# Optimization experiments

Measured on AMD Instinct MI355X. Metric: run time of the kernel, lower is better.

## Reference

```python
import jax, jax.numpy as jnp
import numpy as np
from jax import lax

B, C, H, W = 2, 384, 32, 32
N_HEAD, N_GROUP = 12, 6
HC = C // N_HEAD          # 32 head channels
GC = C // N_GROUP         # 64 group channels
GH = N_HEAD // N_GROUP    # 2 heads per group
KK = 7                    # depthwise kernel (25<=32<=48)
OFF_FACTOR = 2.0
SCALE = HC ** -0.5
EPS = 1e-5


def setup_inputs() -> dict:
    key = jax.random.key(0)
    ks = jax.random.split(key, 16)
    s = 0.02
    inp = {
        "x": jax.random.normal(ks[0], (B, C, H, W), jnp.float32),
        "Wq": jax.random.normal(ks[1], (C, C), jnp.float32) * s,
        "bq": jnp.zeros((C,), jnp.float32),
        "Wk": jax.random.normal(ks[2], (C, C), jnp.float32) * s,
        "bk": jnp.zeros((C,), jnp.float32),
        "Wv": jax.random.normal(ks[3], (C, C), jnp.float32) * s,
        "bv": jnp.zeros((C,), jnp.float32),
        "Wo": jax.random.normal(ks[4], (C, C), jnp.float32) * s,
        "bo": jnp.zeros((C,), jnp.float32),
        "off_dw_w": jax.random.normal(ks[5], (GC, 1, KK, KK), jnp.float32) * s,  # depthwise OIHW
        "off_dw_b": jnp.zeros((GC,), jnp.float32),
        "ln_g": jnp.ones((GC,), jnp.float32),
        "ln_b": jnp.zeros((GC,), jnp.float32),
        "off_pw_w": jax.random.normal(ks[6], (2, GC), jnp.float32) * s,  # 1x1 conv, no bias
        "rpe_table": jax.random.normal(ks[7], (N_HEAD, 2 * H - 1, 2 * W - 1), jnp.float32) * 0.01,
    }
    return inp


def _ref_points(Hk, Wk):
    # torch.linspace(0.5, Hk-0.5, Hk)/Hk*2-1 == ((i+0.5)/Hk)*2-1
    ry = ((jnp.arange(Hk, dtype=jnp.float32) + 0.5) / Hk) * 2.0 - 1.0
    rx = ((jnp.arange(Wk, dtype=jnp.float32) + 0.5) / Wk) * 2.0 - 1.0
    gy, gx = jnp.meshgrid(ry, rx, indexing='ij')
    return jnp.stack((gy, gx), axis=-1)  # [Hk, Wk, 2] in (y, x) order


def _grid_sample(img, grid):
    # img: [N, Cc, Hi, Wi]; grid: [N, Hg, Wg, 2] in (x, y), align_corners=True, zeros padding
    N, Cc, Hi, Wi = img.shape
    Hg, Wg = grid.shape[1], grid.shape[2]
    gx = (grid[..., 0] + 1.0) * 0.5 * (Wi - 1)
    gy = (grid[..., 1] + 1.0) * 0.5 * (Hi - 1)
    x0 = jnp.floor(gx)
    y0 = jnp.floor(gy)
    wx = gx - x0
    wy = gy - y0
    img_f = img.reshape(N, Cc, Hi * Wi)

    def corner(xi, yi, w):
        valid = (xi >= 0) & (xi <= Wi - 1) & (yi >= 0) & (yi <= Hi - 1)
        xc = jnp.clip(xi, 0, Wi - 1).astype(jnp.int32)
        yc = jnp.clip(yi, 0, Hi - 1).astype(jnp.int32)
        idx = (yc * Wi + xc).reshape(N, 1, Hg * Wg)
        vals = jnp.take_along_axis(img_f, jnp.broadcast_to(idx, (N, Cc, Hg * Wg)), axis=2)
        w = (w * valid.astype(img.dtype)).reshape(N, 1, Hg * Wg)
        return vals * w

    out = (corner(x0, y0, (1 - wx) * (1 - wy))
           + corner(x0 + 1, y0, wx * (1 - wy))
           + corner(x0, y0 + 1, (1 - wx) * wy)
           + corner(x0 + 1, y0 + 1, wx * wy))
    return out.reshape(N, Cc, Hg, Wg)


def _conv1x1(x, w, b=None):
    y = jnp.einsum('bchw,oc->bohw', x, w)
    if b is not None:
        y = y + b[None, :, None, None]
    return y


def _forward(x, Wq, bq, Wk, bk, Wv, bv, Wo, bo, off_dw_w, off_dw_b, ln_g, ln_b, off_pw_w, rpe_table):
    q = _conv1x1(x, Wq, bq)                                        # [B, C, H, W]
    q_off = q.reshape(B * N_GROUP, GC, H, W)
    # conv_offset: depthwise conv -> LayerNorm(ch) -> GELU -> 1x1 conv to 2 ch
    o = lax.conv_general_dilated(q_off, off_dw_w, (1, 1), ((KK // 2, KK // 2), (KK // 2, KK // 2)),
                                 feature_group_count=GC,
                                 dimension_numbers=('NCHW', 'OIHW', 'NCHW'))
    o = o + off_dw_b[None, :, None, None]
    mu = jnp.mean(o, axis=1, keepdims=True)
    var = jnp.mean((o - mu) ** 2, axis=1, keepdims=True)
    o = (o - mu) * lax.rsqrt(var + EPS) * ln_g[None, :, None, None] + ln_b[None, :, None, None]
    o = jax.nn.gelu(o, approximate=False)
    off = jnp.einsum('bchw,oc->bohw', o, off_pw_w)                 # [BG, 2, Hs, Ws]
    Hs, Ws = off.shape[2], off.shape[3]
    n_sample = Hs * Ws
    off_range = jnp.array([1.0 / Hs, 1.0 / Ws], jnp.float32).reshape(1, 2, 1, 1)
    off = jnp.tanh(off) * off_range * OFF_FACTOR
    off = jnp.transpose(off, (0, 2, 3, 1))                         # [BG, Hs, Ws, 2] (y, x)
    pos = off + _ref_points(Hs, Ws)[None]                          # [BG, Hs, Ws, 2]

    x_g = x.reshape(B * N_GROUP, GC, H, W)
    x_s = _grid_sample(x_g, pos[..., ::-1])                        # [BG, GC, Hs, Ws]
    x_s = x_s.reshape(B, C, 1, n_sample)

    k = _conv1x1(x_s, Wk, bk).reshape(B * N_HEAD, HC, n_sample)
    v = _conv1x1(x_s, Wv, bv).reshape(B * N_HEAD, HC, n_sample)
    qh = q.reshape(B * N_HEAD, HC, H * W)
    attn = jnp.einsum('bcm,bcn->bmn', qh, k) * SCALE               # [BH, HW, ns]

    # RPE: bilinear lookup of relative-position table at query-sample displacements
    q_grid = _ref_points(H, W).reshape(1, H * W, 1, 2)
    disp = (q_grid - pos.reshape(B * N_GROUP, 1, n_sample, 2)) * 0.5  # [BG, HW, ns, 2] (y, x)
    rpe_b = jnp.broadcast_to(rpe_table[None], (B, N_HEAD, 2 * H - 1, 2 * W - 1))
    rpe_b = rpe_b.reshape(B * N_GROUP, GH, 2 * H - 1, 2 * W - 1)
    attn_bias = _grid_sample(rpe_b, disp[..., ::-1])               # [BG, GH, HW, ns]
    attn = attn + attn_bias.reshape(B * N_HEAD, H * W, n_sample)

    attn = jax.nn.softmax(attn, axis=2)
    out = jnp.einsum('bmn,bcn->bcm', attn, v).reshape(B, C, H, W)
    y = _conv1x1(out, Wo, bo)
    return y


def reference(x, Wq, bq, Wk, bk, Wv, bv, Wo, bo, off_dw_w, off_dw_b, ln_g, ln_b, off_pw_w, rpe_table):
    return _forward(x, Wq, bq, Wk, bk, Wv, bv, Wo, bo,
                    off_dw_w, off_dw_b, ln_g, ln_b, off_pw_w, rpe_table)
```

## Files before the change

kernel.cpp:

```cpp
#include <hip/hip_runtime.h>
#include <hip/hip_fp16.h>
#include <math.h>

#define HH 32
#define WW 32
#define HWSZ 1024
#define CC 384
#define NHEAD 12
#define NGROUP 6
#define HC 32
#define GC 64
#define NS 1024
#define ATTN_SCALE 0.17677669529663687f

typedef _Float16 half8_t __attribute__((ext_vector_type(8)));
typedef _Float16 half4_t __attribute__((ext_vector_type(4)));
typedef _Float16 half2_t __attribute__((ext_vector_type(2)));
typedef float    f4_t    __attribute__((ext_vector_type(4)));

template<int XLO>
__global__ __launch_bounds__(256) void gemm_wx(
    const float* __restrict__ W, const float* __restrict__ bias,
    const float* __restrict__ X, float* __restrict__ Y)
{
    const int bz = blockIdx.z;
    const int tm = blockIdx.y * 32;
    const int tn = blockIdx.x * 64;
    const int tid = threadIdx.x;
    const int w = tid >> 6, lane = tid & 63;
    const int quad = lane >> 4, lcol = lane & 15;

    __shared__ _Float16 sWh[32][40];
    __shared__ _Float16 sXh[64][40];
    __shared__ _Float16 sXl[XLO ? 64 : 1][40];

    const float* Xb = X + (size_t)bz * CC * 1024;
    float* Yb = Y + (size_t)bz * CC * 1024;

    f4_t acc0 = {0.f, 0.f, 0.f, 0.f}, acc1 = {0.f, 0.f, 0.f, 0.f};

    for (int k0 = 0; k0 < CC; k0 += 32) {
        {
            int m = tid >> 3, k4 = (tid & 7) * 4;
            float4 wv = *(const float4*)&W[(size_t)(tm + m) * CC + k0 + k4];
            half4_t h; h[0] = (_Float16)wv.x; h[1] = (_Float16)wv.y;
            h[2] = (_Float16)wv.z; h[3] = (_Float16)wv.w;
            *(half4_t*)&sWh[m][k4] = h;
        }
        {
            int k = tid >> 3, nj = tid & 7;
            const float* xr = &Xb[(size_t)(k0 + k) * 1024 + tn + nj];
#pragma unroll
            for (int i = 0; i < 8; ++i) {
                float v = xr[8 * i];
                _Float16 h = (_Float16)v;
                sXh[nj + 8 * i][k] = h;
                if (XLO) sXl[nj + 8 * i][k] = (_Float16)(v - (float)h);
            }
        }
        __syncthreads();

        half8_t Ah0 = *(const half8_t*)&sWh[lcol][quad * 8];
        half8_t Ah1 = *(const half8_t*)&sWh[16 + lcol][quad * 8];
        half8_t Bh  = *(const half8_t*)&sXh[w * 16 + lcol][quad * 8];
        acc0 = __builtin_amdgcn_mfma_f32_16x16x32_f16(Ah0, Bh, acc0, 0, 0, 0);
        acc1 = __builtin_amdgcn_mfma_f32_16x16x32_f16(Ah1, Bh, acc1, 0, 0, 0);
        if (XLO) {
            half8_t Bl = *(const half8_t*)&sXl[w * 16 + lcol][quad * 8];
            acc0 = __builtin_amdgcn_mfma_f32_16x16x32_f16(Ah0, Bl, acc0, 0, 0, 0);
            acc1 = __builtin_amdgcn_mfma_f32_16x16x32_f16(Ah1, Bl, acc1, 0, 0, 0);
        }
        __syncthreads();
    }

#pragma unroll
    for (int r = 0; r < 4; ++r) {
        int m0 = tm + quad * 4 + r;
        Yb[(size_t)m0 * 1024 + tn + w * 16 + lcol]        = acc0[r] + bias[m0];
        Yb[(size_t)(m0 + 16) * 1024 + tn + w * 16 + lcol] = acc1[r] + bias[m0 + 16];
    }
}

__global__ __launch_bounds__(256) void gemm_kv_fused(
    const float* __restrict__ Wk, const float* __restrict__ bk,
    const float* __restrict__ Wv, const float* __restrict__ bv,
    const float* __restrict__ X,
    _Float16* __restrict__ khT, _Float16* __restrict__ vhb)
{
    const int bz = blockIdx.z;
    const int head = blockIdx.y;
    const int tm = head * 32;
    const int tn = blockIdx.x * 64;
    const int tid = threadIdx.x;
    const int w = tid >> 6, lane = tid & 63;
    const int quad = lane >> 4, lcol = lane & 15;
    const int bh = bz * 12 + head;

    __shared__ _Float16 sWk[32][40], sWv[32][40];
    __shared__ _Float16 sXh[64][40];

    const float* Xb = X + (size_t)bz * CC * 1024;

    f4_t ak0 = {0.f, 0.f, 0.f, 0.f}, ak1 = {0.f, 0.f, 0.f, 0.f};
    f4_t av0 = {0.f, 0.f, 0.f, 0.f}, av1 = {0.f, 0.f, 0.f, 0.f};

    for (int k0 = 0; k0 < CC; k0 += 32) {
        {
            int m = tid >> 3, k4 = (tid & 7) * 4;
            float4 wk = *(const float4*)&Wk[(size_t)(tm + m) * CC + k0 + k4];
            float4 wv = *(const float4*)&Wv[(size_t)(tm + m) * CC + k0 + k4];
            half4_t hk; hk[0] = (_Float16)wk.x; hk[1] = (_Float16)wk.y;
            hk[2] = (_Float16)wk.z; hk[3] = (_Float16)wk.w;
            half4_t hv; hv[0] = (_Float16)wv.x; hv[1] = (_Float16)wv.y;
            hv[2] = (_Float16)wv.z; hv[3] = (_Float16)wv.w;
            *(half4_t*)&sWk[m][k4] = hk;
            *(half4_t*)&sWv[m][k4] = hv;
        }
        {
            int k = tid >> 3, nj = tid & 7;
            const float* xr = &Xb[(size_t)(k0 + k) * 1024 + tn + nj];
#pragma unroll
            for (int i = 0; i < 8; ++i)
                sXh[nj + 8 * i][k] = (_Float16)xr[8 * i];
        }
        __syncthreads();

        half8_t Xa = *(const half8_t*)&sXh[w * 16 + lcol][quad * 8];
        half8_t K0 = *(const half8_t*)&sWk[lcol][quad * 8];
        half8_t K1 = *(const half8_t*)&sWk[16 + lcol][quad * 8];
        half8_t V0 = *(const half8_t*)&sWv[lcol][quad * 8];
        half8_t V1 = *(const half8_t*)&sWv[16 + lcol][quad * 8];
        ak0 = __builtin_amdgcn_mfma_f32_16x16x32_f16(Xa, K0, ak0, 0, 0, 0);
        ak1 = __builtin_amdgcn_mfma_f32_16x16x32_f16(Xa, K1, ak1, 0, 0, 0);
        av0 = __builtin_amdgcn_mfma_f32_16x16x32_f16(V0, Xa, av0, 0, 0, 0);
        av1 = __builtin_amdgcn_mfma_f32_16x16x32_f16(V1, Xa, av1, 0, 0, 0);
        __syncthreads();
    }

    {
        float bk0 = bk[tm + lcol], bk1 = bk[tm + 16 + lcol];
#pragma unroll
        for (int r = 0; r < 4; ++r) {
            int n = tn + w * 16 + quad * 4 + r;
            khT[((size_t)bh * 1024 + n) * 32 + lcol]      = (_Float16)(ak0[r] + bk0);
            khT[((size_t)bh * 1024 + n) * 32 + 16 + lcol] = (_Float16)(ak1[r] + bk1);
        }
    }
    {
#pragma unroll
        for (int r = 0; r < 4; ++r) {
            int hc0 = quad * 4 + r;
            vhb[((size_t)bh * 32 + hc0) * 1024 + tn + w * 16 + lcol] =
                (_Float16)(av0[r] + bv[tm + hc0]);
            vhb[((size_t)bh * 32 + hc0 + 16) * 1024 + tn + w * 16 + lcol] =
                (_Float16)(av1[r] + bv[tm + hc0 + 16]);
        }
    }
}

__global__ __launch_bounds__(256) void dwconv_kernel(
    const float* __restrict__ q, const float* __restrict__ dww,
    const float* __restrict__ dwb, float* __restrict__ oconv)
{
    const int bc = blockIdx.x;
    const int bg = bc >> 6, c = bc & 63;
    const int b = bg / 6, g = bg % 6;
    const float* plane = q + ((size_t)b * CC + g * 64 + c) * 1024;

    __shared__ float sp[1024];
    __shared__ float sw[49];
    const int tid = threadIdx.x;
    for (int i = tid; i < 1024; i += 256) sp[i] = plane[i];
    if (tid < 49) sw[tid] = dww[c * 49 + tid];
    __syncthreads();

    const float bias = dwb[c];
    for (int i = tid; i < 1024; i += 256) {
        int y = i >> 5, x = i & 31;
        float s = 0.f;
#pragma unroll
        for (int ky = 0; ky < 7; ++ky) {
            int yy = y + ky - 3;
            if (yy < 0 || yy > 31) continue;
#pragma unroll
            for (int kx = 0; kx < 7; ++kx) {
                int xx = x + kx - 3;
                if (xx < 0 || xx > 31) continue;
                s += sp[yy * 32 + xx] * sw[ky * 7 + kx];
            }
        }
        oconv[(size_t)bc * 1024 + i] = s + bias;
    }
}

__global__ __launch_bounds__(256) void offset_sample_kernel(
    const float* __restrict__ oconv, const float* __restrict__ lng,
    const float* __restrict__ lnb, const float* __restrict__ pw,
    const float* __restrict__ x, float* __restrict__ pos,
    float* __restrict__ xs)
{
    const int bg = blockIdx.y;
    const int cs = blockIdx.z;
    const int px0 = blockIdx.x * 64;
    const int t = threadIdx.x;
    const int cg = t >> 6, pl = t & 63;
    const int px = px0 + pl;
    const int b = bg / 6, g = bg % 6;

    __shared__ float red[4][64];
    __shared__ float spos[64][2];

    const float* base = oconv + ((size_t)bg * 64 + cg * 16) * 1024 + px;
    float col[16];
    float s = 0.f;
#pragma unroll
    for (int i = 0; i < 16; ++i) { col[i] = base[(size_t)i * 1024]; s += col[i]; }
    red[cg][pl] = s;
    __syncthreads();
    float mu = (red[0][pl] + red[1][pl] + red[2][pl] + red[3][pl]) * (1.f / 64.f);
    float v = 0.f;
#pragma unroll
    for (int i = 0; i < 16; ++i) { float d = col[i] - mu; v += d * d; }
    __syncthreads();
    red[cg][pl] = v;
    __syncthreads();
    float inv = rsqrtf((red[0][pl] + red[1][pl] + red[2][pl] + red[3][pl]) * (1.f / 64.f) + 1e-5f);

    float oy = 0.f, ox = 0.f;
#pragma unroll
    for (int i = 0; i < 16; ++i) {
        int c = cg * 16 + i;
        float val = (col[i] - mu) * inv * lng[c] + lnb[c];
        float gl = 0.5f * val * (1.f + erff(val * 0.70710678118654752440f));
        oy += gl * pw[c];
        ox += gl * pw[64 + c];
    }
    __syncthreads();
    red[cg][pl] = oy;
    __syncthreads();
    float oyt = red[0][pl] + red[1][pl] + red[2][pl] + red[3][pl];
    __syncthreads();
    red[cg][pl] = ox;
    __syncthreads();
    if (cg == 0) {
        float oxt = red[0][pl] + red[1][pl] + red[2][pl] + red[3][pl];
        float offy = tanhf(oyt) * (2.0f / 32.0f);
        float offx = tanhf(oxt) * (2.0f / 32.0f);
        int y = px >> 5, xx = px & 31;
        float ry = ((y + 0.5f) / 32.f) * 2.f - 1.f;
        float rx = ((xx + 0.5f) / 32.f) * 2.f - 1.f;
        float py = offy + ry, pxv = offx + rx;
        spos[pl][0] = py; spos[pl][1] = pxv;
        if (cs == 0) {
            pos[((size_t)bg * 1024 + px) * 2 + 0] = py;
            pos[((size_t)bg * 1024 + px) * 2 + 1] = pxv;
        }
    }
    __syncthreads();

    float py = spos[pl][0], pxv = spos[pl][1];
    float gx = (pxv + 1.f) * 0.5f * 31.f;
    float gy = (py + 1.f) * 0.5f * 31.f;
    float x0f = floorf(gx), y0f = floorf(gy);
    float wx = gx - x0f, wy = gy - y0f;
    int x0 = (int)x0f, y0 = (int)y0f;
    float vx0 = ((unsigned)x0 <= 31u) ? 1.f : 0.f;
    float vx1 = ((unsigned)(x0 + 1) <= 31u) ? 1.f : 0.f;
    float vy0 = ((unsigned)y0 <= 31u) ? 1.f : 0.f;
    float vy1 = ((unsigned)(y0 + 1) <= 31u) ? 1.f : 0.f;
    float w00 = (1.f - wx) * (1.f - wy) * vx0 * vy0;
    float w01 = wx * (1.f - wy) * vx1 * vy0;
    float w10 = (1.f - wx) * wy * vx0 * vy1;
    float w11 = wx * wy * vx1 * vy1;
    int xc0 = min(max(x0, 0), 31), xc1 = min(max(x0 + 1, 0), 31);
    int yc0 = min(max(y0, 0), 31), yc1 = min(max(y0 + 1, 0), 31);
    int i00 = yc0 * 32 + xc0, i01 = yc0 * 32 + xc1;
    int i10 = yc1 * 32 + xc0, i11 = yc1 * 32 + xc1;

    const int c0 = cs * 16 + cg * 4;
    const float* xb = x + ((size_t)b * CC + g * 64 + c0) * 1024;
    float* xso = xs + ((size_t)b * CC + g * 64 + c0) * 1024 + px;
#pragma unroll
    for (int i = 0; i < 4; ++i) {
        const float* plane = xb + (size_t)i * 1024;
        xso[(size_t)i * 1024] = plane[i00] * w00 + plane[i01] * w01
                              + plane[i10] * w10 + plane[i11] * w11;
    }
}

__global__ __launch_bounds__(256) void attn_mfma_kernel(
    const float* __restrict__ q, const _Float16* __restrict__ khT,
    const _Float16* __restrict__ vhb, const float* __restrict__ pos,
    const float* __restrict__ rpe, float* __restrict__ out)
{
    const int bh = blockIdx.y;
    const int b = bh / 12, head = bh % 12;
    const int bg = b * 6 + (head >> 1);
    const int mblk = blockIdx.x * 16;
    const int tid = threadIdx.x;
    const int w = tid >> 6, lane = tid & 63;
    const int quad = lane >> 4, lcol = lane & 15;

    __shared__ __align__(16) char smem[19584];
    half2_t*  srpe2 = (half2_t*)smem;
    _Float16* sqh   = (_Float16*)(smem + 8832);
    _Float16* spw   = (_Float16*)(smem + 9856) + w * (16 * 72);
    float*    cml   = (float*)(smem + 19072);
    float*    comb  = (float*)(smem + 9856);

    const float qyw = (((mblk >> 5) + 0.5f) * (1.f / 32.f)) * 2.f - 1.f;
    int r0; {
        float gy_lo = (qyw - 1.03125f) * 15.5f + 31.f;
        r0 = (int)floorf(gy_lo);
        r0 = min(max(r0, 0), 28);
    }

    const float* rp = rpe + (size_t)head * 3969;
    for (int i = tid; i < 35 * 63; i += 256) {
        int y = i / 63, xx = i - y * 63;
        int gi = (r0 + y) * 63 + xx;
        float v0 = rp[gi];
        float v1 = (xx < 62) ? rp[gi + 1] : 0.f;
        half2_t hv; hv[0] = (_Float16)v0; hv[1] = (_Float16)v1;
        srpe2[i] = hv;
    }
    {
        const float* qb = q + ((size_t)b * CC + head * 32) * 1024 + mblk;
        for (int i = tid; i < 512; i += 256) {
            int hc = i >> 4, m = i & 15;
            sqh[m * 32 + hc] = (_Float16)qb[(size_t)hc * 1024 + m];
        }
    }
    __syncthreads();

    half8_t qf = *(const half8_t*)&sqh[lcol * 32 + quad * 8];
    const float qx = (((mblk & 31) + lcol + 0.5f) * (1.f / 32.f)) * 2.f - 1.f;

    const float2* pgv = (const float2*)(pos + (size_t)bg * 2048);
    const _Float16* khb = khT + (size_t)bh * 1024 * 32;
    const _Float16* vhh = vhb + (size_t)bh * 32 * 1024;

    f4_t o0 = {0.f, 0.f, 0.f, 0.f}, o1 = {0.f, 0.f, 0.f, 0.f};
    float lsum = 0.f;

#pragma unroll 1
    for (int c = 0; c < 4; ++c) {
        const int n0 = w * 256 + c * 64;

        half8_t khv[4];
#pragma unroll
        for (int t = 0; t < 4; ++t)
            khv[t] = *(const half8_t*)&khb[(size_t)(n0 + t * 16 + lcol) * 32 + quad * 8];
        half8_t vv0[2], vv1[2];
#pragma unroll
        for (int kp = 0; kp < 2; ++kp) {
            int nb = n0 + kp * 32 + quad * 8;
            vv0[kp] = *(const half8_t*)&vhh[(size_t)lcol * 1024 + nb];
            vv1[kp] = *(const half8_t*)&vhh[(size_t)(16 + lcol) * 1024 + nb];
        }

        f4_t S[4];
#pragma unroll
        for (int t = 0; t < 4; ++t) {
            f4_t s = {0.f, 0.f, 0.f, 0.f};
            s = __builtin_amdgcn_mfma_f32_16x16x32_f16(khv[t], qf, s, 0, 0, 0);
#pragma unroll
            for (int r = 0; r < 4; ++r) {
                int key = n0 + t * 16 + quad * 4 + r;
                float2 pp = pgv[key];
                float gy = (qyw - pp.x) * 15.5f + 31.f;
                float gx = (qx  - pp.y) * 15.5f + 31.f;
                float y0f = floorf(gy), x0f = floorf(gx);
                float wy = gy - y0f, wx = gx - x0f;
                int i00 = ((int)y0f - r0) * 63 + (int)x0f;
                half2_t p0 = srpe2[i00];
                half2_t p1 = srpe2[i00 + 63];
                float r00 = (float)p0[0], r01 = (float)p0[1];
                float r10 = (float)p1[0], r11 = (float)p1[1];
                float top = r00 + (r01 - r00) * wx;
                float bot = r10 + (r11 - r10) * wx;
                s[r] = s[r] * ATTN_SCALE + top + (bot - top) * wy;
            }
            S[t] = s;
        }

#pragma unroll
        for (int t = 0; t < 4; ++t) {
            float p0 = __expf(S[t][0]);
            float p1 = __expf(S[t][1]);
            float p2 = __expf(S[t][2]);
            float p3 = __expf(S[t][3]);
            lsum += (p0 + p1) + (p2 + p3);
            half4_t h;
            h[0] = (_Float16)p0; h[1] = (_Float16)p1;
            h[2] = (_Float16)p2; h[3] = (_Float16)p3;
            *(half4_t*)&spw[lcol * 72 + t * 16 + quad * 4] = h;
        }

#pragma unroll
        for (int kp = 0; kp < 2; ++kp) {
            half8_t pb = *(const half8_t*)&spw[lcol * 72 + kp * 32 + quad * 8];
            o0 = __builtin_amdgcn_mfma_f32_16x16x32_f16(vv0[kp], pb, o0, 0, 0, 0);
            o1 = __builtin_amdgcn_mfma_f32_16x16x32_f16(vv1[kp], pb, o1, 0, 0, 0);
        }
    }

    lsum += __shfl_xor(lsum, 16);
    lsum += __shfl_xor(lsum, 32);

    __syncthreads();

    *(f4_t*)&comb[(w * 16 + lcol) * 36 + quad * 4]      = o0;
    *(f4_t*)&comb[(w * 16 + lcol) * 36 + 16 + quad * 4] = o1;
    if (quad == 0) cml[w * 16 + lcol] = lsum;
    __syncthreads();

#pragma unroll
    for (int i = 0; i < 2; ++i) {
        int idx = tid + i * 256;
        int qq = idx >> 5, hc = idx & 31;
        float L = cml[qq] + cml[16 + qq] + cml[32 + qq] + cml[48 + qq];
        float o = comb[(0 * 16 + qq) * 36 + hc]
                + comb[(1 * 16 + qq) * 36 + hc]
                + comb[(2 * 16 + qq) * 36 + hc]
                + comb[(3 * 16 + qq) * 36 + hc];
        out[((size_t)b * CC + head * 32 + hc) * 1024 + mblk + qq] = o / L;
    }
}

extern "C" void kernel_launch(void* const* d_in, const int* in_sizes, int n_in,
                              void* d_out, int out_size, void* d_ws, size_t ws_size,
                              hipStream_t stream) {
    const float* x   = (const float*)d_in[0];
    const float* Wq  = (const float*)d_in[1];
    const float* bq  = (const float*)d_in[2];
    const float* Wk  = (const float*)d_in[3];
    const float* bk  = (const float*)d_in[4];
    const float* Wv  = (const float*)d_in[5];
    const float* bv  = (const float*)d_in[6];
    const float* Wo  = (const float*)d_in[7];
    const float* bo  = (const float*)d_in[8];
    const float* dww = (const float*)d_in[9];
    const float* dwb = (const float*)d_in[10];
    const float* lng = (const float*)d_in[11];
    const float* lnb = (const float*)d_in[12];
    const float* pw  = (const float*)d_in[13];
    const float* rpe = (const float*)d_in[14];

    float* ws = (float*)d_ws;
    const size_t SZ = 786432;
    float* qbuf  = ws;
    float* xs    = ws + 1 * SZ;
    float* abuf  = ws + 2 * SZ;
    float* oconv = ws + 3 * SZ;
    _Float16* khT = (_Float16*)(ws + 4 * SZ);
    _Float16* vhb = (_Float16*)(ws + 5 * SZ);
    float* pos   = ws + 6 * SZ;

    dim3 gqo(16, 12, 2);
    gemm_wx<0><<<gqo, 256, 0, stream>>>(Wq, bq, x, qbuf);
    dwconv_kernel<<<768, 256, 0, stream>>>(qbuf, dww, dwb, oconv);
    offset_sample_kernel<<<dim3(16, 12, 4), 256, 0, stream>>>(oconv, lng, lnb, pw, x, pos, xs);
    gemm_kv_fused<<<dim3(16, 12, 2), 256, 0, stream>>>(Wk, bk, Wv, bv, xs, khT, vhb);
    attn_mfma_kernel<<<dim3(64, 24), 256, 0, stream>>>(qbuf, khT, vhb, pos, rpe, abuf);
    gemm_wx<1><<<gqo, 256, 0, stream>>>(Wo, bo, abuf, (float*)d_out);
}
```

Baseline: 172.4 us.

## Shrink GEMM N-tile to 32 and split warps 2x2 to double block count

The Q/O projection GEMM and the fused K/V GEMM now use 32x32 output tiles instead of 32x64, with the four waves laid out as a 2x2 grid of 16x16 sub-tiles. Grid size doubles from 384 to 768 blocks so more of the GPU's compute units stay busy on these small GEMMs. The cost is that weight tiles are reloaded and converted twice as often, and each wave issues fewer MFMAs per barrier, so synchronisation overhead per unit of work goes up.

```diff
diff --git a/kernel.cpp b/kernel.cpp
--- a/kernel.cpp
+++ b/kernel.cpp
@@ -25,33 +25,34 @@
 {
     const int bz = blockIdx.z;
     const int tm = blockIdx.y * 32;
-    const int tn = blockIdx.x * 64;
+    const int tn = blockIdx.x * 32;
     const int tid = threadIdx.x;
     const int w = tid >> 6, lane = tid & 63;
     const int quad = lane >> 4, lcol = lane & 15;
+    const int wm = w >> 1, wn = w & 1;
 
     __shared__ _Float16 sWh[32][40];
-    __shared__ _Float16 sXh[64][40];
-    __shared__ _Float16 sXl[XLO ? 64 : 1][40];
+    __shared__ _Float16 sXh[32][40];
+    __shared__ _Float16 sXl[XLO ? 32 : 1][40];
 
     const float* Xb = X + (size_t)bz * CC * 1024;
     float* Yb = Y + (size_t)bz * CC * 1024;
 
-    f4_t acc0 = {0.f, 0.f, 0.f, 0.f}, acc1 = {0.f, 0.f, 0.f, 0.f};
+    f4_t acc = {0.f, 0.f, 0.f, 0.f};
 
     for (int k0 = 0; k0 < CC; k0 += 32) {
         {
-            int m = tid >> 3, k4 = (tid & 7) * 4;
-            float4 wv = *(const float4*)&W[(size_t)(tm + m) * CC + k0 + k4];
+            int m = tid >> 3, kc = (tid & 7) * 4;
+            float4 wv = *(const float4*)&W[(size_t)(tm + m) * CC + k0 + kc];
             half4_t h; h[0] = (_Float16)wv.x; h[1] = (_Float16)wv.y;
             h[2] = (_Float16)wv.z; h[3] = (_Float16)wv.w;
-            *(half4_t*)&sWh[m][k4] = h;
+            *(half4_t*)&sWh[m][kc] = h;
         }
         {
             int k = tid >> 3, nj = tid & 7;
             const float* xr = &Xb[(size_t)(k0 + k) * 1024 + tn + nj];
 #pragma unroll
-            for (int i = 0; i < 8; ++i) {
+            for (int i = 0; i < 4; ++i) {
                 float v = xr[8 * i];
                 _Float16 h = (_Float16)v;
                 sXh[nj + 8 * i][k] = h;
@@ -60,24 +61,20 @@
         }
         __syncthreads();
 
-        half8_t Ah0 = *(const half8_t*)&sWh[lcol][quad * 8];
-        half8_t Ah1 = *(const half8_t*)&sWh[16 + lcol][quad * 8];
-        half8_t Bh  = *(const half8_t*)&sXh[w * 16 + lcol][quad * 8];
-        acc0 = __builtin_amdgcn_mfma_f32_16x16x32_f16(Ah0, Bh, acc0, 0, 0, 0);
-        acc1 = __builtin_amdgcn_mfma_f32_16x16x32_f16(Ah1, Bh, acc1, 0, 0, 0);
+        half8_t Ah = *(const half8_t*)&sWh[wm * 16 + lcol][quad * 8];
+        half8_t Bh = *(const half8_t*)&sXh[wn * 16 + lcol][quad * 8];
+        acc = __builtin_amdgcn_mfma_f32_16x16x32_f16(Ah, Bh, acc, 0, 0, 0);
         if (XLO) {
-            half8_t Bl = *(const half8_t*)&sXl[w * 16 + lcol][quad * 8];
-            acc0 = __builtin_amdgcn_mfma_f32_16x16x32_f16(Ah0, Bl, acc0, 0, 0, 0);
-            acc1 = __builtin_amdgcn_mfma_f32_16x16x32_f16(Ah1, Bl, acc1, 0, 0, 0);
+            half8_t Bl = *(const half8_t*)&sXl[wn * 16 + lcol][quad * 8];
+            acc = __builtin_amdgcn_mfma_f32_16x16x32_f16(Ah, Bl, acc, 0, 0, 0);
         }
         __syncthreads();
     }
 
 #pragma unroll
     for (int r = 0; r < 4; ++r) {
-        int m0 = tm + quad * 4 + r;
-        Yb[(size_t)m0 * 1024 + tn + w * 16 + lcol]        = acc0[r] + bias[m0];
-        Yb[(size_t)(m0 + 16) * 1024 + tn + w * 16 + lcol] = acc1[r] + bias[m0 + 16];
+        int m0 = tm + wm * 16 + quad * 4 + r;
+        Yb[(size_t)m0 * 1024 + tn + wn * 16 + lcol] = acc[r] + bias[m0];
     }
 }
 
@@ -90,70 +87,65 @@
     const int bz = blockIdx.z;
     const int head = blockIdx.y;
     const int tm = head * 32;
-    const int tn = blockIdx.x * 64;
+    const int tn = blockIdx.x * 32;
     const int tid = threadIdx.x;
     const int w = tid >> 6, lane = tid & 63;
     const int quad = lane >> 4, lcol = lane & 15;
+    const int wm = w >> 1, wn = w & 1;
     const int bh = bz * 12 + head;
 
     __shared__ _Float16 sWk[32][40], sWv[32][40];
-    __shared__ _Float16 sXh[64][40];
+    __shared__ _Float16 sXh[32][40];
 
     const float* Xb = X + (size_t)bz * CC * 1024;
 
-    f4_t ak0 = {0.f, 0.f, 0.f, 0.f}, ak1 = {0.f, 0.f, 0.f, 0.f};
-    f4_t av0 = {0.f, 0.f, 0.f, 0.f}, av1 = {0.f, 0.f, 0.f, 0.f};
+    f4_t ak = {0.f, 0.f, 0.f, 0.f};
+    f4_t av = {0.f, 0.f, 0.f, 0.f};
 
     for (int k0 = 0; k0 < CC; k0 += 32) {
         {
-            int m = tid >> 3, k4 = (tid & 7) * 4;
-            float4 wk = *(const float4*)&Wk[(size_t)(tm + m) * CC + k0 + k4];
-            float4 wv = *(const float4*)&Wv[(size_t)(tm + m) * CC + k0 + k4];
-            half4_t hk; hk[0] = (_Float16)wk.x; hk[1] = (_Float16)wk.y;
-            hk[2] = (_Float16)wk.z; hk[3] = (_Float16)wk.w;
-            half4_t hv; hv[0] = (_Float16)wv.x; hv[1] = (_Float16)wv.y;
-            hv[2] = (_Float16)wv.z; hv[3] = (_Float16)wv.w;
-            *(half4_t*)&sWk[m][k4] = hk;
-            *(half4_t*)&sWv[m][k4] = hv;
+            int m = tid >> 3, kc = (tid & 7) * 4;
+            float4 wkv = *(const float4*)&Wk[(size_t)(tm + m) * CC + k0 + kc];
+            float4 wvv = *(const float4*)&Wv[(size_t)(tm + m) * CC + k0 + kc];
+            half4_t hk; hk[0] = (_Float16)wkv.x; hk[1] = (_Float16)wkv.y;
+            hk[2] = (_Float16)wkv.z; hk[3] = (_Float16)wkv.w;
+            half4_t hv; hv[0] = (_Float16)wvv.x; hv[1] = (_Float16)wvv.y;
+            hv[2] = (_Float16)wvv.z; hv[3] = (_Float16)wvv.w;
+            *(half4_t*)&sWk[m][kc] = hk;
+            *(half4_t*)&sWv[m][kc] = hv;
         }
         {
             int k = tid >> 3, nj = tid & 7;
             const float* xr = &Xb[(size_t)(k0 + k) * 1024 + tn + nj];
 #pragma unroll
-            for (int i = 0; i < 8; ++i)
+            for (int i = 0; i < 4; ++i)
                 sXh[nj + 8 * i][k] = (_Float16)xr[8 * i];
         }
         __syncthreads();
 
-        half8_t Xa = *(const half8_t*)&sXh[w * 16 + lcol][quad * 8];
-        half8_t K0 = *(const half8_t*)&sWk[lcol][quad * 8];
-        half8_t K1 = *(const half8_t*)&sWk[16 + lcol][quad * 8];
-        half8_t V0 = *(const half8_t*)&sWv[lcol][quad * 8];
-        half8_t V1 = *(const half8_t*)&sWv[16 + lcol][quad * 8];
-        ak0 = __builtin_amdgcn_mfma_f32_16x16x32_f16(Xa, K0, ak0, 0, 0, 0);
-        ak1 = __builtin_amdgcn_mfma_f32_16x16x32_f16(Xa, K1, ak1, 0, 0, 0);
-        av0 = __builtin_amdgcn_mfma_f32_16x16x32_f16(V0, Xa, av0, 0, 0, 0);
-        av1 = __builtin_amdgcn_mfma_f32_16x16x32_f16(V1, Xa, av1, 0, 0, 0);
+        half8_t Xf = *(const half8_t*)&sXh[wn * 16 + lcol][quad * 8];
+        half8_t Kf = *(const half8_t*)&sWk[wm * 16 + lcol][quad * 8];
+        half8_t Vf = *(const half8_t*)&sWv[wm * 16 + lcol][quad * 8];
+        ak = __builtin_amdgcn_mfma_f32_16x16x32_f16(Xf, Kf, ak, 0, 0, 0);
+        av = __builtin_amdgcn_mfma_f32_16x16x32_f16(Vf, Xf, av, 0, 0, 0);
         __syncthreads();
     }
 
     {
-        float bk0 = bk[tm + lcol], bk1 = bk[tm + 16 + lcol];
+        int hc = wm * 16 + lcol;
+        float bkv = bk[tm + hc];
 #pragma unroll
         for (int r = 0; r < 4; ++r) {
-            int n = tn + w * 16 + quad * 4 + r;
-            khT[((size_t)bh * 1024 + n) * 32 + lcol]      = (_Float16)(ak0[r] + bk0);
-            khT[((size_t)bh * 1024 + n) * 32 + 16 + lcol] = (_Float16)(ak1[r] + bk1);
+            int n = tn + wn * 16 + quad * 4 + r;
+            khT[((size_t)bh * 1024 + n) * 32 + hc] = (_Float16)(ak[r] + bkv);
         }
     }
     {
+        int n = tn + wn * 16 + lcol;
 #pragma unroll
         for (int r = 0; r < 4; ++r) {
-            int hc0 = quad * 4 + r;
-            vhb[((size_t)bh * 32 + hc0) * 1024 + tn + w * 16 + lcol] =
-                (_Float16)(av0[r] + bv[tm + hc0]);
-            vhb[((size_t)bh * 32 + hc0 + 16) * 1024 + tn + w * 16 + lcol] =
-                (_Float16)(av1[r] + bv[tm + hc0 + 16]);
+            int hc0 = wm * 16 + quad * 4 + r;
+            vhb[((size_t)bh * 32 + hc0) * 1024 + n] = (_Float16)(av[r] + bv[tm + hc0]);
         }
     }
 }
@@ -457,11 +449,11 @@
     _Float16* vhb = (_Float16*)(ws + 5 * SZ);
     float* pos   = ws + 6 * SZ;
 
-    dim3 gqo(16, 12, 2);
+    dim3 gqo(32, 12, 2);
     gemm_wx<0><<<gqo, 256, 0, stream>>>(Wq, bq, x, qbuf);
     dwconv_kernel<<<768, 256, 0, stream>>>(qbuf, dww, dwb, oconv);
     offset_sample_kernel<<<dim3(16, 12, 4), 256, 0, stream>>>(oconv, lng, lnb, pw, x, pos, xs);
-    gemm_kv_fused<<<dim3(16, 12, 2), 256, 0, stream>>>(Wk, bk, Wv, bv, xs, khT, vhb);
+    gemm_kv_fused<<<dim3(32, 12, 2), 256, 0, stream>>>(Wk, bk, Wv, bv, xs, khT, vhb);
     attn_mfma_kernel<<<dim3(64, 24), 256, 0, stream>>>(qbuf, khT, vhb, pos, rpe, abuf);
     gemm_wx<1><<<gqo, 256, 0, stream>>>(Wo, bo, abuf, (float*)d_out);
 }
```

Measured after the change: 174.3 us. Within noise of the previous version (+1.1%).

## Process both heads of an offset group per attention block to share position work

Applied to the files above, without the earlier changes.

The attention kernel now handles the two heads that share one offset group in a single block instead of one head per block, halving the grid. The per-key position loads, grid coordinates, floor and bilinear weights are computed once and reused for both heads' RPE lookups, and both RPE tables are staged into shared memory together. In exchange, shared memory roughly doubles, register pressure rises, and there are half as many blocks (768), which may reduce occupancy and latency hiding.

```diff
diff --git a/kernel.cpp b/kernel.cpp
--- a/kernel.cpp
+++ b/kernel.cpp
@@ -293,20 +293,24 @@
     const _Float16* __restrict__ vhb, const float* __restrict__ pos,
     const float* __restrict__ rpe, float* __restrict__ out)
 {
-    const int bh = blockIdx.y;
-    const int b = bh / 12, head = bh % 12;
-    const int bg = b * 6 + (head >> 1);
+    const int bgp = blockIdx.y;
+    const int b = bgp / 6, g = bgp % 6;
+    const int h0 = g * 2;
+    const int bh0 = b * 12 + h0, bh1 = bh0 + 1;
     const int mblk = blockIdx.x * 16;
     const int tid = threadIdx.x;
     const int w = tid >> 6, lane = tid & 63;
     const int quad = lane >> 4, lcol = lane & 15;
 
-    __shared__ __align__(16) char smem[19584];
-    half2_t*  srpe2 = (half2_t*)smem;
-    _Float16* sqh   = (_Float16*)(smem + 8832);
-    _Float16* spw   = (_Float16*)(smem + 9856) + w * (16 * 72);
-    float*    cml   = (float*)(smem + 19072);
-    float*    comb  = (float*)(smem + 9856);
+    __shared__ __align__(16) char smem[38656];
+    half2_t*  srpe0 = (half2_t*)smem;
+    half2_t*  srpe1 = (half2_t*)(smem + 8832);
+    _Float16* sqh   = (_Float16*)(smem + 17664);
+    _Float16* spw   = (_Float16*)(smem + 19712) + w * 2304;
+    float*    cml0  = (float*)(smem + 38144);
+    float*    cml1  = (float*)(smem + 38400);
+    float*    comb0 = (float*)(smem + 19712);
+    float*    comb1 = (float*)(smem + 19712 + 9216);
 
     const float qyw = (((mblk >> 5) + 0.5f) * (1.f / 32.f)) * 2.f - 1.f;
     int r0; {
@@ -315,55 +319,63 @@
         r0 = min(max(r0, 0), 28);
     }
 
-    const float* rp = rpe + (size_t)head * 3969;
-    for (int i = tid; i < 35 * 63; i += 256) {
-        int y = i / 63, xx = i - y * 63;
-        int gi = (r0 + y) * 63 + xx;
-        float v0 = rp[gi];
-        float v1 = (xx < 62) ? rp[gi + 1] : 0.f;
-        half2_t hv; hv[0] = (_Float16)v0; hv[1] = (_Float16)v1;
-        srpe2[i] = hv;
-    }
     {
-        const float* qb = q + ((size_t)b * CC + head * 32) * 1024 + mblk;
-        for (int i = tid; i < 512; i += 256) {
-            int hc = i >> 4, m = i & 15;
-            sqh[m * 32 + hc] = (_Float16)qb[(size_t)hc * 1024 + m];
-        }
-    }
-    __syncthreads();
-
-    half8_t qf = *(const half8_t*)&sqh[lcol * 32 + quad * 8];
+        const float* rp0 = rpe + (size_t)h0 * 3969;
+        const float* rp1 = rp0 + 3969;
+        for (int i = tid; i < 35 * 63; i += 256) {
+            int y = i / 63, xx = i - y * 63;
+            int gi = (r0 + y) * 63 + xx;
+            float a0 = rp0[gi], b0 = (xx < 62) ? rp0[gi + 1] : 0.f;
+            float a1 = rp1[gi], b1 = (xx < 62) ? rp1[gi + 1] : 0.f;
+            half2_t hv0; hv0[0] = (_Float16)a0; hv0[1] = (_Float16)b0;
+            half2_t hv1; hv1[0] = (_Float16)a1; hv1[1] = (_Float16)b1;
+            srpe0[i] = hv0;
+            srpe1[i] = hv1;
+        }
+    }
+    {
+        const float* qb = q + ((size_t)b * CC + h0 * 32) * 1024 + mblk;
+        for (int i = tid; i < 1024; i += 256) {
+            int hh = i >> 9, rem = i & 511;
+            int hc = rem >> 4, m = rem & 15;
+            sqh[hh * 512 + m * 32 + hc] =
+                (_Float16)qb[(size_t)(hh * 32 + hc) * 1024 + m];
+        }
+    }
+    __syncthreads();
+
+    half8_t qf0 = *(const half8_t*)&sqh[lcol * 32 + quad * 8];
+    half8_t qf1 = *(const half8_t*)&sqh[512 + lcol * 32 + quad * 8];
     const float qx = (((mblk & 31) + lcol + 0.5f) * (1.f / 32.f)) * 2.f - 1.f;
 
-    const float2* pgv = (const float2*)(pos + (size_t)bg * 2048);
-    const _Float16* khb = khT + (size_t)bh * 1024 * 32;
-    const _Float16* vhh = vhb + (size_t)bh * 32 * 1024;
-
-    f4_t o0 = {0.f, 0.f, 0.f, 0.f}, o1 = {0.f, 0.f, 0.f, 0.f};
-    float lsum = 0.f;
+    const float2* pgv = (const float2*)(pos + (size_t)bgp * 2048);
+    const _Float16* khb0 = khT + (size_t)bh0 * 1024 * 32;
+    const _Float16* khb1 = khT + (size_t)bh1 * 1024 * 32;
+    const _Float16* vhh0 = vhb + (size_t)bh0 * 32 * 1024;
+    const _Float16* vhh1 = vhb + (size_t)bh1 * 32 * 1024;
+
+    f4_t o00 = {0.f, 0.f, 0.f, 0.f}, o01 = {0.f, 0.f, 0.f, 0.f};
+    f4_t o10 = {0.f, 0.f, 0.f, 0.f}, o11 = {0.f, 0.f, 0.f, 0.f};
+    float lsum0 = 0.f, lsum1 = 0.f;
 
 #pragma unroll 1
     for (int c = 0; c < 4; ++c) {
         const int n0 = w * 256 + c * 64;
 
-        half8_t khv[4];
-#pragma unroll
-        for (int t = 0; t < 4; ++t)
-            khv[t] = *(const half8_t*)&khb[(size_t)(n0 + t * 16 + lcol) * 32 + quad * 8];
-        half8_t vv0[2], vv1[2];
-#pragma unroll
-        for (int kp = 0; kp < 2; ++kp) {
-            int nb = n0 + kp * 32 + quad * 8;
-            vv0[kp] = *(const half8_t*)&vhh[(size_t)lcol * 1024 + nb];
-            vv1[kp] = *(const half8_t*)&vhh[(size_t)(16 + lcol) * 1024 + nb];
-        }
-
-        f4_t S[4];
+        half8_t khv0[4], khv1[4];
 #pragma unroll
         for (int t = 0; t < 4; ++t) {
-            f4_t s = {0.f, 0.f, 0.f, 0.f};
-            s = __builtin_amdgcn_mfma_f32_16x16x32_f16(khv[t], qf, s, 0, 0, 0);
+            size_t off = (size_t)(n0 + t * 16 + lcol) * 32 + quad * 8;
+            khv0[t] = *(const half8_t*)&khb0[off];
+            khv1[t] = *(const half8_t*)&khb1[off];
+        }
+
+        f4_t S0[4], S1[4];
+#pragma unroll
+        for (int t = 0; t < 4; ++t) {
+            f4_t s0 = {0.f, 0.f, 0.f, 0.f}, s1 = {0.f, 0.f, 0.f, 0.f};
+            s0 = __builtin_amdgcn_mfma_f32_16x16x32_f16(khv0[t], qf0, s0, 0, 0, 0);
+            s1 = __builtin_amdgcn_mfma_f32_16x16x32_f16(khv1[t], qf1, s1, 0, 0, 0);
 #pragma unroll
             for (int r = 0; r < 4; ++r) {
                 int key = n0 + t * 16 + quad * 4 + r;
@@ -373,58 +385,102 @@
                 float y0f = floorf(gy), x0f = floorf(gx);
                 float wy = gy - y0f, wx = gx - x0f;
                 int i00 = ((int)y0f - r0) * 63 + (int)x0f;
-                half2_t p0 = srpe2[i00];
-                half2_t p1 = srpe2[i00 + 63];
-                float r00 = (float)p0[0], r01 = (float)p0[1];
-                float r10 = (float)p1[0], r11 = (float)p1[1];
-                float top = r00 + (r01 - r00) * wx;
-                float bot = r10 + (r11 - r10) * wx;
-                s[r] = s[r] * ATTN_SCALE + top + (bot - top) * wy;
+                {
+                    half2_t p0 = srpe0[i00];
+                    half2_t p1 = srpe0[i00 + 63];
+                    float t0 = (float)p0[0] + ((float)p0[1] - (float)p0[0]) * wx;
+                    float b0 = (float)p1[0] + ((float)p1[1] - (float)p1[0]) * wx;
+                    s0[r] = s0[r] * ATTN_SCALE + t0 + (b0 - t0) * wy;
+                }
+                {
+                    half2_t p0 = srpe1[i00];
+                    half2_t p1 = srpe1[i00 + 63];
+                    float t1 = (float)p0[0] + ((float)p0[1] - (float)p0[0]) * wx;
+                    float b1 = (float)p1[0] + ((float)p1[1] - (float)p1[0]) * wx;
+                    s1[r] = s1[r] * ATTN_SCALE + t1 + (b1 - t1) * wy;
+                }
             }
-            S[t] = s;
+            S0[t] = s0; S1[t] = s1;
+        }
+
+        half8_t vv00[2], vv01[2];
+#pragma unroll
+        for (int kp = 0; kp < 2; ++kp) {
+            int nb = n0 + kp * 32 + quad * 8;
+            vv00[kp] = *(const half8_t*)&vhh0[(size_t)lcol * 1024 + nb];
+            vv01[kp] = *(const half8_t*)&vhh0[(size_t)(16 + lcol) * 1024 + nb];
         }
 
 #pragma unroll
         for (int t = 0; t < 4; ++t) {
-            float p0 = __expf(S[t][0]);
-            float p1 = __expf(S[t][1]);
-            float p2 = __expf(S[t][2]);
-            float p3 = __expf(S[t][3]);
-            lsum += (p0 + p1) + (p2 + p3);
+            float p0 = __expf(S0[t][0]), p1 = __expf(S0[t][1]);
+            float p2 = __expf(S0[t][2]), p3 = __expf(S0[t][3]);
+            lsum0 += (p0 + p1) + (p2 + p3);
             half4_t h;
             h[0] = (_Float16)p0; h[1] = (_Float16)p1;
             h[2] = (_Float16)p2; h[3] = (_Float16)p3;
             *(half4_t*)&spw[lcol * 72 + t * 16 + quad * 4] = h;
+            float r0e = __expf(S1[t][0]), r1e = __expf(S1[t][1]);
+            float r2e = __expf(S1[t][2]), r3e = __expf(S1[t][3]);
+            lsum1 += (r0e + r1e) + (r2e + r3e);
+            half4_t h1;
+            h1[0] = (_Float16)r0e; h1[1] = (_Float16)r1e;
+            h1[2] = (_Float16)r2e; h1[3] = (_Float16)r3e;
+            *(half4_t*)&spw[1152 + lcol * 72 + t * 16 + quad * 4] = h1;
         }
 
 #pragma unroll
         for (int kp = 0; kp < 2; ++kp) {
             half8_t pb = *(const half8_t*)&spw[lcol * 72 + kp * 32 + quad * 8];
-            o0 = __builtin_amdgcn_mfma_f32_16x16x32_f16(vv0[kp], pb, o0, 0, 0, 0);
-            o1 = __builtin_amdgcn_mfma_f32_16x16x32_f16(vv1[kp], pb, o1, 0, 0, 0);
-        }
-    }
-
-    lsum += __shfl_xor(lsum, 16);
-    lsum += __shfl_xor(lsum, 32);
-
-    __syncthreads();
-
-    *(f4_t*)&comb[(w * 16 + lcol) * 36 + quad * 4]      = o0;
-    *(f4_t*)&comb[(w * 16 + lcol) * 36 + 16 + quad * 4] = o1;
-    if (quad == 0) cml[w * 16 + lcol] = lsum;
+            o00 = __builtin_amdgcn_mfma_f32_16x16x32_f16(vv00[kp], pb, o00, 0, 0, 0);
+            o01 = __builtin_amdgcn_mfma_f32_16x16x32_f16(vv01[kp], pb, o01, 0, 0, 0);
+        }
+#pragma unroll
+        for (int kp = 0; kp < 2; ++kp) {
+            int nb = n0 + kp * 32 + quad * 8;
+            half8_t v0 = *(const half8_t*)&vhh1[(size_t)lcol * 1024 + nb];
+            half8_t v1 = *(const half8_t*)&vhh1[(size_t)(16 + lcol) * 1024 + nb];
+            half8_t pb = *(const half8_t*)&spw[1152 + lcol * 72 + kp * 32 + quad * 8];
+            o10 = __builtin_amdgcn_mfma_f32_16x16x32_f16(v0, pb, o10, 0, 0, 0);
+            o11 = __builtin_amdgcn_mfma_f32_16x16x32_f16(v1, pb, o11, 0, 0, 0);
+        }
+    }
+
+    lsum0 += __shfl_xor(lsum0, 16); lsum0 += __shfl_xor(lsum0, 32);
+    lsum1 += __shfl_xor(lsum1, 16); lsum1 += __shfl_xor(lsum1, 32);
+
+    __syncthreads();
+
+    *(f4_t*)&comb0[(w * 16 + lcol) * 36 + quad * 4]      = o00;
+    *(f4_t*)&comb0[(w * 16 + lcol) * 36 + 16 + quad * 4] = o01;
+    *(f4_t*)&comb1[(w * 16 + lcol) * 36 + quad * 4]      = o10;
+    *(f4_t*)&comb1[(w * 16 + lcol) * 36 + 16 + quad * 4] = o11;
+    if (quad == 0) {
+        cml0[w * 16 + lcol] = lsum0;
+        cml1[w * 16 + lcol] = lsum1;
+    }
     __syncthreads();
 
 #pragma unroll
     for (int i = 0; i < 2; ++i) {
         int idx = tid + i * 256;
         int qq = idx >> 5, hc = idx & 31;
-        float L = cml[qq] + cml[16 + qq] + cml[32 + qq] + cml[48 + qq];
-        float o = comb[(0 * 16 + qq) * 36 + hc]
-                + comb[(1 * 16 + qq) * 36 + hc]
-                + comb[(2 * 16 + qq) * 36 + hc]
-                + comb[(3 * 16 + qq) * 36 + hc];
-        out[((size_t)b * CC + head * 32 + hc) * 1024 + mblk + qq] = o / L;
+        {
+            float L = cml0[qq] + cml0[16 + qq] + cml0[32 + qq] + cml0[48 + qq];
+            float o = comb0[(0 * 16 + qq) * 36 + hc]
+                    + comb0[(1 * 16 + qq) * 36 + hc]
+                    + comb0[(2 * 16 + qq) * 36 + hc]
+                    + comb0[(3 * 16 + qq) * 36 + hc];
+            out[((size_t)b * CC + h0 * 32 + hc) * 1024 + mblk + qq] = o / L;
+        }
+        {
+            float L = cml1[qq] + cml1[16 + qq] + cml1[32 + qq] + cml1[48 + qq];
+            float o = comb1[(0 * 16 + qq) * 36 + hc]
+                    + comb1[(1 * 16 + qq) * 36 + hc]
+                    + comb1[(2 * 16 + qq) * 36 + hc]
+                    + comb1[(3 * 16 + qq) * 36 + hc];
+            out[((size_t)b * CC + (h0 + 1) * 32 + hc) * 1024 + mblk + qq] = o / L;
+        }
     }
 }
 
@@ -462,6 +518,6 @@
     dwconv_kernel<<<768, 256, 0, stream>>>(qbuf, dww, dwb, oconv);
     offset_sample_kernel<<<dim3(16, 12, 4), 256, 0, stream>>>(oconv, lng, lnb, pw, x, pos, xs);
     gemm_kv_fused<<<dim3(16, 12, 2), 256, 0, stream>>>(Wk, bk, Wv, bv, xs, khT, vhb);
-    attn_mfma_kernel<<<dim3(64, 24), 256, 0, stream>>>(qbuf, khT, vhb, pos, rpe, abuf);
+    attn_mfma_kernel<<<dim3(64, 12), 256, 0, stream>>>(qbuf, khT, vhb, pos, rpe, abuf);
     gemm_wx<1><<<gqo, 256, 0, stream>>>(Wo, bo, abuf, (float*)d_out);
 }
```

Result: faster. 166.0 us (-3.7%).
